# Kernel tuning notes

Hardware: AMD Instinct MI355X
Metric: run time of the kernel (lower is better)

The kernel has to match this reference:

```python
import jax, jax.numpy as jnp
import numpy as np

N_NODES = 64000
N_GRAPHS = 128


def _sage_conv(x, edge_index, Wl, Wr, b):
    # PyG SAGEConv (mean aggregator): out = lin_l(mean_{j in N(i)} x_j) + lin_r(x_i)
    src, dst = edge_index[0], edge_index[1]
    msg = x[src]                                   # [E, d] gather
    s = jax.ops.segment_sum(msg, dst, num_segments=N_NODES)          # [N, d]
    cnt = jax.ops.segment_sum(jnp.ones(src.shape, x.dtype), dst,
                              num_segments=N_NODES)[:, None]          # [N, 1]
    aggr = jnp.where(cnt > 0, s / jnp.maximum(cnt, 1.0), jnp.zeros((), x.dtype))
    return aggr @ Wl.T + x @ Wr.T + b


def setup_inputs() -> dict:
    key = jax.random.key(0)
    ks = jax.random.split(key, 9)
    E = 1024000
    x = jax.random.normal(ks[0], (N_NODES, 64), dtype=jnp.float32)
    edge_index = jax.random.randint(ks[1], (2, E), 0, N_NODES, dtype=jnp.int64)
    batch = jnp.sort(jax.random.randint(ks[2], (N_NODES,), 0, N_GRAPHS, dtype=jnp.int64))
    sc = 1.0 / np.sqrt(64.0)
    Wl = jax.random.normal(ks[3], (3, 64, 64), dtype=jnp.float32) * sc
    Wr = jax.random.normal(ks[4], (3, 64, 64), dtype=jnp.float32) * sc
    b = jax.random.normal(ks[5], (3, 64), dtype=jnp.float32) * sc
    Wl_out = jax.random.normal(ks[6], (2, 64), dtype=jnp.float32) * sc
    Wr_out = jax.random.normal(ks[7], (2, 64), dtype=jnp.float32) * sc
    b_out = jax.random.normal(ks[8], (2,), dtype=jnp.float32) * sc
    return {"x": x, "edge_index": edge_index, "batch": batch,
            "Wl": Wl, "Wr": Wr, "b": b,
            "Wl_out": Wl_out, "Wr_out": Wr_out, "b_out": b_out}


def reference(x, edge_index, batch, Wl, Wr, b, Wl_out, Wr_out, b_out):
    h = x
    for i in range(Wl.shape[0]):  # fixed n_layers=3 hidden SAGEConv layers
        h = _sage_conv(h, edge_index, Wl[i], Wr[i], b[i])
        # dropout is identity at inference
        h = jax.nn.relu(h)
    h = _sage_conv(h, edge_index, Wl_out, Wr_out, b_out)  # [N, n_classes]
    # global mean pool over graphs in the batch
    s = jax.ops.segment_sum(h, batch, num_segments=N_GRAPHS)
    cnt = jax.ops.segment_sum(jnp.ones((N_NODES,), h.dtype), batch,
                              num_segments=N_GRAPHS)[:, None]
    return s / jnp.maximum(cnt, 1.0)
```

## Files before the change

### kernel.cpp

```cpp
#include <hip/hip_runtime.h>

#define NNODES 64000
#define NGRAPHS 128
#define D 64
#define NT 250
#define ESEG 5120

typedef _Float16 half8 __attribute__((ext_vector_type(8)));
typedef float f32x4 __attribute__((ext_vector_type(4)));

__device__ __forceinline__ int lower_bound(const int* __restrict__ a, int n, int key) {
    int lo = 0, hi = n;
    while (lo < hi) {
        int mid = (lo + hi) >> 1;
        if (a[mid] < key) lo = mid + 1; else hi = mid;
    }
    return lo;
}


__global__ void tohalf_kernel(const float4* __restrict__ x, half8* __restrict__ xh, int n8,
                              const float* __restrict__ Wl, const float* __restrict__ Wr,
                              _Float16* __restrict__ Wlh, _Float16* __restrict__ Wrh) {
    int i = blockIdx.x * blockDim.x + threadIdx.x;
    int st = gridDim.x * blockDim.x;
    for (; i < n8; i += st) {
        float4 a = x[2 * i], b = x[2 * i + 1];
        half8 o;
        o[0] = (_Float16)a.x; o[1] = (_Float16)a.y; o[2] = (_Float16)a.z; o[3] = (_Float16)a.w;
        o[4] = (_Float16)b.x; o[5] = (_Float16)b.y; o[6] = (_Float16)b.z; o[7] = (_Float16)b.w;
        xh[i] = o;
    }
    int j = blockIdx.x * blockDim.x + threadIdx.x;
    if (j < 3 * D * D) {
        Wlh[j] = (_Float16)Wl[j];
        Wrh[j] = (_Float16)Wr[j];
    }
}

__global__ __launch_bounds__(256) void partition_kernel(
        const int* __restrict__ src, const int* __restrict__ dst, int E,
        int* __restrict__ ecur, int2* __restrict__ elist) {
    __shared__ int bcnt[256], bbase[256];
    const int U = 8;
    int tid = threadIdx.x;
    for (int base = blockIdx.x * 256 * U; base < E; base += gridDim.x * 256 * U) {
        bcnt[tid] = 0;
        __syncthreads();
        int2 ed[U]; int team[U], slot[U];
#pragma unroll
        for (int u = 0; u < U; ++u) {
            int e = base + tid + u * 256;
            team[u] = -1;
            if (e < E) {
                int s = __builtin_nontemporal_load(src + e);
                int d = __builtin_nontemporal_load(dst + e);
                ed[u] = make_int2(s, d);
                team[u] = d >> 8;
                slot[u] = atomicAdd(&bcnt[team[u]], 1);
            }
        }
        __syncthreads();
        if (bcnt[tid] > 0) bbase[tid] = atomicAdd(&ecur[tid], bcnt[tid]);
        __syncthreads();
#pragma unroll
        for (int u = 0; u < U; ++u)
            if (team[u] >= 0)
                elist[(size_t)team[u] * ESEG + bbase[team[u]] + slot[u]] = ed[u];
        __syncthreads();
    }
}

__global__ void teamscan_kernel(const int* __restrict__ ecur, int* __restrict__ tbase,
                                int* __restrict__ offs) {
    __shared__ int s[256];
    int t = threadIdx.x;
    int v = (t < NT) ? ecur[t] : 0;
    s[t] = v;
    __syncthreads();
    for (int off = 1; off < 256; off <<= 1) {
        int x = (t >= off) ? s[t - off] : 0;
        __syncthreads();
        s[t] += x;
        __syncthreads();
    }
    if (t < NT) tbase[t] = s[t] - v;
    if (t == 255) offs[NNODES] = s[255];
}

__global__ __launch_bounds__(1024) void fill_block(
        const int2* __restrict__ elist, const int* __restrict__ ecur,
        const int* __restrict__ tbase, const int* __restrict__ batch,
        int* __restrict__ offs, int2* __restrict__ info, int* __restrict__ col) {
    __shared__ int lhist[256], lofs[256];
    int team = blockIdx.x;
    int t = threadIdx.x;
    int n = ecur[team];
    int tb = tbase[team];
    const int2* el = elist + (size_t)team * ESEG;
    if (t < 256) lhist[t] = 0;
    __syncthreads();
    for (int e = t; e < n; e += 1024)
        atomicAdd(&lhist[el[e].y & 255], 1);
    __syncthreads();
    if (t < 256) lofs[t] = lhist[t];
    __syncthreads();
    for (int off = 1; off < 256; off <<= 1) {
        int x = 0;
        if (t < 256 && t >= off) x = lofs[t - off];
        __syncthreads();
        if (t < 256) lofs[t] += x;
        __syncthreads();
    }
    if (t < 256) {
        int v = lhist[t];
        int ex = lofs[t] - v;
        int gi = team * 256 + t;
        offs[gi] = tb + ex;
        float inv = (v > 0) ? 1.f / (float)v : 0.f;
        info[gi] = make_int2(batch[gi], __float_as_int(inv));
        lofs[t] = ex;
    }
    __syncthreads();
    for (int e = t; e < n; e += 1024) {
        int2 ed = el[e];
        int p = tb + atomicAdd(&lofs[ed.y & 255], 1);
        col[p] = ed.x;
    }
}

template <int PRJ>
__global__ __launch_bounds__(256) void layer_fused(
        const _Float16* __restrict__ h, _Float16* __restrict__ out,
        const int* __restrict__ offs, const int* __restrict__ col,
        const _Float16* __restrict__ Wlh, const _Float16* __restrict__ Wrh,
        const float* __restrict__ b,
        const float* __restrict__ Wlo, const float* __restrict__ Wro,
        float* __restrict__ z12, float* __restrict__ z34) {
    __shared__ _Float16 tile[4][16][D];
    int lane = threadIdx.x & 63;
    int w    = threadIdx.x >> 6;
    int row0 = (blockIdx.x * 4 + w) * 16;

    int ns = lane >> 3;
    int ch = lane & 7;
#pragma unroll
    for (int pass = 0; pass < 2; ++pass) {
        int i = row0 + pass * 8 + ns;
        int beg = offs[i], end = offs[i + 1];
        float s[8] = {0.f, 0.f, 0.f, 0.f, 0.f, 0.f, 0.f, 0.f};
        int e = beg;
        for (; e + 8 <= end; e += 8) {
            int c[8];
#pragma unroll
            for (int u = 0; u < 8; ++u) c[u] = col[e + u];
            half8 v[8];
#pragma unroll
            for (int u = 0; u < 8; ++u)
                v[u] = *(const half8*)(h + (size_t)c[u] * D + ch * 8);
#pragma unroll
            for (int u = 0; u < 8; ++u)
#pragma unroll
                for (int j = 0; j < 8; ++j) s[j] += (float)v[u][j];
        }
        for (; e + 4 <= end; e += 4) {
            int c0 = col[e], c1 = col[e + 1], c2 = col[e + 2], c3 = col[e + 3];
            half8 v0 = *(const half8*)(h + (size_t)c0 * D + ch * 8);
            half8 v1 = *(const half8*)(h + (size_t)c1 * D + ch * 8);
            half8 v2 = *(const half8*)(h + (size_t)c2 * D + ch * 8);
            half8 v3 = *(const half8*)(h + (size_t)c3 * D + ch * 8);
#pragma unroll
            for (int j = 0; j < 8; ++j)
                s[j] += ((float)v0[j] + (float)v1[j]) + ((float)v2[j] + (float)v3[j]);
        }
        for (; e < end; ++e) {
            half8 v = *(const half8*)(h + (size_t)col[e] * D + ch * 8);
#pragma unroll
            for (int j = 0; j < 8; ++j) s[j] += (float)v[j];
        }
        float inv = (end > beg) ? 1.f / (float)(end - beg) : 0.f;
        half8 o;
#pragma unroll
        for (int j = 0; j < 8; ++j) o[j] = (_Float16)(s[j] * inv);
        *(half8*)(&tile[w][pass * 8 + ns][ch * 8]) = o;
    }

    int r = lane & 15;
    int g = lane >> 4;

    half8 bf[4][4];
#pragma unroll
    for (int kt = 0; kt < 4; ++kt) {
        const _Float16* Wm = (kt < 2) ? Wlh : Wrh;
        int kk = (kt & 1) * 32 + g * 8;
#pragma unroll
        for (int nt = 0; nt < 4; ++nt)
            bf[kt][nt] = *(const half8*)(Wm + (size_t)(nt * 16 + r) * D + kk);
    }

    f32x4 acc[4];
#pragma unroll
    for (int nt = 0; nt < 4; ++nt) {
        float bv = b[nt * 16 + r];
        acc[nt] = (f32x4){bv, bv, bv, bv};
    }

#pragma unroll
    for (int kt = 0; kt < 4; ++kt) {
        int kk = (kt & 1) * 32 + g * 8;
        half8 af;
        if (kt < 2) af = *(const half8*)(&tile[w][r][kk]);
        else        af = *(const half8*)(h + (size_t)(row0 + r) * D + kk);
#pragma unroll
        for (int nt = 0; nt < 4; ++nt)
            acc[nt] = __builtin_amdgcn_mfma_f32_16x16x32_f16(af, bf[kt][nt], acc[nt], 0, 0, 0);
    }

    if (!PRJ) {
#pragma unroll
        for (int nt = 0; nt < 4; ++nt)
#pragma unroll
            for (int q = 0; q < 4; ++q) {
                int row = row0 + g * 4 + q;
                out[(size_t)row * D + nt * 16 + r] = (_Float16)fmaxf(acc[nt][q], 0.f);
            }
    } else {
#pragma unroll
        for (int nt = 0; nt < 4; ++nt)
#pragma unroll
            for (int q = 0; q < 4; ++q)
                tile[w][g * 4 + q][nt * 16 + r] = (_Float16)fmaxf(acc[nt][q], 0.f);

        half8 pf[2];
#pragma unroll
        for (int kt = 0; kt < 2; ++kt) {
            half8 t = {0, 0, 0, 0, 0, 0, 0, 0};
            if (r < 4) {
                const float* Pr = (r < 2) ? (Wlo + r * D) : (Wro + (r - 2) * D);
                int kk = kt * 32 + g * 8;
#pragma unroll
                for (int j = 0; j < 8; ++j) t[j] = (_Float16)Pr[kk + j];
            }
            pf[kt] = t;
        }
        f32x4 az = (f32x4){0.f, 0.f, 0.f, 0.f};
#pragma unroll
        for (int kt = 0; kt < 2; ++kt) {
            half8 af = *(const half8*)(&tile[w][r][kt * 32 + g * 8]);
            az = __builtin_amdgcn_mfma_f32_16x16x32_f16(af, pf[kt], az, 0, 0, 0);
        }
#pragma unroll
        for (int q = 0; q < 4; ++q) {
            int row = row0 + g * 4 + q;
            if (r < 2)      z12[row * 2 + r]       = az[q];
            else if (r < 4) z34[row * 2 + (r - 2)] = az[q];
        }
    }
}

__global__ __launch_bounds__(256) void zpool_edge(
        const float2* __restrict__ z12, const float2* __restrict__ z34,
        const int* __restrict__ src, const int* __restrict__ dst,
        const int2* __restrict__ info, int E, float* __restrict__ pool) {
    __shared__ float lp[NGRAPHS * 2];
    int t = threadIdx.x;
    lp[t] = 0.f;
    __syncthreads();
    int tid = blockIdx.x * blockDim.x + t;
    int stride = gridDim.x * blockDim.x;
    for (int e = tid; e < E; e += stride) {
        int s = __builtin_nontemporal_load(src + e);
        int d = __builtin_nontemporal_load(dst + e);
        float2 z = z12[s];
        int2 nf = info[d];
        float w = __int_as_float(nf.y);
        atomicAdd(&lp[nf.x * 2 + 0], z.x * w);
        atomicAdd(&lp[nf.x * 2 + 1], z.y * w);
    }
    for (int i = tid; i < NNODES; i += stride) {
        float2 zi = z34[i];
        int g = info[i].x;
        atomicAdd(&lp[g * 2 + 0], zi.x);
        atomicAdd(&lp[g * 2 + 1], zi.y);
    }
    __syncthreads();
    float v = lp[t];
    if (v != 0.f) atomicAdd(&pool[t], v);
}

__global__ void out_kernel(const float* __restrict__ pool, const int* __restrict__ batch,
                           const float* __restrict__ bo, float* __restrict__ out) {
    int t = threadIdx.x;
    int g = t >> 1, j = t & 1;
    int start = lower_bound(batch, NNODES, g);
    int end   = lower_bound(batch, NNODES, g + 1);
    int c = end - start;
    out[t] = (c > 0) ? pool[t] / (float)c + bo[j] : 0.f;
}


extern "C" void kernel_launch(void* const* d_in, const int* in_sizes, int n_in,
                              void* d_out, int out_size, void* d_ws, size_t ws_size,
                              hipStream_t stream) {
    const float* x    = (const float*)d_in[0];
    const int*   eidx = (const int*)d_in[1];
    const int*   batch= (const int*)d_in[2];
    const float* Wl   = (const float*)d_in[3];
    const float* Wr   = (const float*)d_in[4];
    const float* b    = (const float*)d_in[5];
    const float* Wlo  = (const float*)d_in[6];
    const float* Wro  = (const float*)d_in[7];
    const float* bo   = (const float*)d_in[8];

    int E = in_sizes[1] / 2;
    const int* src = eidx;
    const int* dst = eidx + E;

    char* ws = (char*)d_ws;
    size_t hb = (size_t)NNODES * D * 2;
    _Float16* xh   = (_Float16*)ws;
    _Float16* bufA = (_Float16*)(ws + hb);
    char* p = ws + 2 * hb;
    _Float16* Wlh  = (_Float16*)p;  p += 3 * D * D * 2;
    _Float16* Wrh  = (_Float16*)p;  p += 3 * D * D * 2;
    int*    col  = (int*)p;     p += (size_t)E * 4;
    int*    offs = (int*)p;     p += ((size_t)(NNODES + 1) * 4 + 127) / 128 * 128;
    int2*   info = (int2*)p;    p += (size_t)NNODES * 8;
    float*  z12  = (float*)p;   p += (size_t)NNODES * 8;
    float*  z34  = (float*)p;   p += (size_t)NNODES * 8;
    float*  pool = (float*)p;   p += (size_t)NGRAPHS * 2 * 4 + 64;
    int*    ecur = (int*)p;     p += 1024;
    int*    tbase= (int*)p;     p += 1024;
    int2*   elist= (int2*)p;

    hipMemsetAsync(pool, 0, NGRAPHS * 2 * sizeof(float), stream);
    hipMemsetAsync(ecur, 0, NT * sizeof(int), stream);

    tohalf_kernel<<<2000, 256, 0, stream>>>((const float4*)x, (half8*)xh, NNODES * D / 8,
                                            Wl, Wr, Wlh, Wrh);

    partition_kernel<<<512, 256, 0, stream>>>(src, dst, E, ecur, elist);
    teamscan_kernel<<<1, 256, 0, stream>>>(ecur, tbase, offs);
    fill_block<<<NT, 1024, 0, stream>>>(elist, ecur, tbase, batch, offs, info, col);

    layer_fused<0><<<1000, 256, 0, stream>>>(xh,   bufA, offs, col,
                                             Wlh,             Wrh,             b,
                                             nullptr, nullptr, nullptr, nullptr);
    layer_fused<0><<<1000, 256, 0, stream>>>(bufA, xh,   offs, col,
                                             Wlh + D * D,     Wrh + D * D,     b + D,
                                             nullptr, nullptr, nullptr, nullptr);
    layer_fused<1><<<1000, 256, 0, stream>>>(xh,   bufA, offs, col,
                                             Wlh + 2 * D * D, Wrh + 2 * D * D, b + 2 * D,
                                             Wlo, Wro, z12, z34);

    zpool_edge<<<1024, 256, 0, stream>>>((const float2*)z12, (const float2*)z34,
                                         src, dst, info, E, pool);
    out_kernel<<<1, 256, 0, stream>>>(pool, batch, bo, (float*)d_out);
}
```

Measured before the change: 170.3 us.

## Drop memsets and scan kernel, accumulate gathers in fp16, deterministic pool partials

The two memsets are removed: the zeroing of the team counters moves into the tohalf kernel. The separate team-scan kernel is folded into fill_block, where each block redoes the 250-entry scan. Neighbour aggregation in the layer kernel now sums in packed fp16 vectors instead of converting every element to fp32, cutting ALU work in the gather loop but adding rounding and overflow risk for high-degree nodes. zpool_edge now runs with 512 blocks, each writing its partial sums to a buffer that out_kernel reduces serially, replacing the global atomics.

```diff
diff --git a/kernel.cpp b/kernel.cpp
--- a/kernel.cpp
+++ b/kernel.cpp
@@ -5,6 +5,7 @@
 #define D 64
 #define NT 250
 #define ESEG 5120
+#define ZG 512
 
 typedef _Float16 half8 __attribute__((ext_vector_type(8)));
 typedef float f32x4 __attribute__((ext_vector_type(4)));
@@ -21,7 +22,8 @@
 
 __global__ void tohalf_kernel(const float4* __restrict__ x, half8* __restrict__ xh, int n8,
                               const float* __restrict__ Wl, const float* __restrict__ Wr,
-                              _Float16* __restrict__ Wlh, _Float16* __restrict__ Wrh) {
+                              _Float16* __restrict__ Wlh, _Float16* __restrict__ Wrh,
+                              int* __restrict__ ecur) {
     int i = blockIdx.x * blockDim.x + threadIdx.x;
     int st = gridDim.x * blockDim.x;
     for (; i < n8; i += st) {
@@ -36,6 +38,7 @@
         Wlh[j] = (_Float16)Wl[j];
         Wrh[j] = (_Float16)Wr[j];
     }
+    if (blockIdx.x == 0 && threadIdx.x < 256) ecur[threadIdx.x] = 0;
 }
 
 __global__ __launch_bounds__(256) void partition_kernel(
@@ -71,33 +74,29 @@
     }
 }
 
-__global__ void teamscan_kernel(const int* __restrict__ ecur, int* __restrict__ tbase,
-                                int* __restrict__ offs) {
-    __shared__ int s[256];
-    int t = threadIdx.x;
-    int v = (t < NT) ? ecur[t] : 0;
-    s[t] = v;
-    __syncthreads();
-    for (int off = 1; off < 256; off <<= 1) {
-        int x = (t >= off) ? s[t - off] : 0;
-        __syncthreads();
-        s[t] += x;
-        __syncthreads();
-    }
-    if (t < NT) tbase[t] = s[t] - v;
-    if (t == 255) offs[NNODES] = s[255];
-}
-
 __global__ __launch_bounds__(1024) void fill_block(
         const int2* __restrict__ elist, const int* __restrict__ ecur,
-        const int* __restrict__ tbase, const int* __restrict__ batch,
+        const int* __restrict__ batch,
         int* __restrict__ offs, int2* __restrict__ info, int* __restrict__ col) {
     __shared__ int lhist[256], lofs[256];
     int team = blockIdx.x;
     int t = threadIdx.x;
     int n = ecur[team];
-    int tb = tbase[team];
     const int2* el = elist + (size_t)team * ESEG;
+
+    if (t < 256) lofs[t] = (t < NT) ? ecur[t] : 0;
+    __syncthreads();
+    for (int off = 1; off < 256; off <<= 1) {
+        int x = 0;
+        if (t < 256 && t >= off) x = lofs[t - off];
+        __syncthreads();
+        if (t < 256) lofs[t] += x;
+        __syncthreads();
+    }
+    int tb = (team > 0) ? lofs[team - 1] : 0;
+    if (team == NT - 1 && t == 0) offs[NNODES] = lofs[NT - 1];
+    __syncthreads();
+
     if (t < 256) lhist[t] = 0;
     __syncthreads();
     for (int e = t; e < n; e += 1024)
@@ -148,7 +147,7 @@
     for (int pass = 0; pass < 2; ++pass) {
         int i = row0 + pass * 8 + ns;
         int beg = offs[i], end = offs[i + 1];
-        float s[8] = {0.f, 0.f, 0.f, 0.f, 0.f, 0.f, 0.f, 0.f};
+        half8 sa = {0, 0, 0, 0, 0, 0, 0, 0};
         int e = beg;
         for (; e + 8 <= end; e += 8) {
             int c[8];
@@ -158,10 +157,9 @@
 #pragma unroll
             for (int u = 0; u < 8; ++u)
                 v[u] = *(const half8*)(h + (size_t)c[u] * D + ch * 8);
-#pragma unroll
-            for (int u = 0; u < 8; ++u)
-#pragma unroll
-                for (int j = 0; j < 8; ++j) s[j] += (float)v[u][j];
+            half8 t0 = v[0] + v[1], t1 = v[2] + v[3];
+            half8 t2 = v[4] + v[5], t3 = v[6] + v[7];
+            sa += (t0 + t1) + (t2 + t3);
         }
         for (; e + 4 <= end; e += 4) {
             int c0 = col[e], c1 = col[e + 1], c2 = col[e + 2], c3 = col[e + 3];
@@ -169,19 +167,14 @@
             half8 v1 = *(const half8*)(h + (size_t)c1 * D + ch * 8);
             half8 v2 = *(const half8*)(h + (size_t)c2 * D + ch * 8);
             half8 v3 = *(const half8*)(h + (size_t)c3 * D + ch * 8);
-#pragma unroll
-            for (int j = 0; j < 8; ++j)
-                s[j] += ((float)v0[j] + (float)v1[j]) + ((float)v2[j] + (float)v3[j]);
-        }
-        for (; e < end; ++e) {
-            half8 v = *(const half8*)(h + (size_t)col[e] * D + ch * 8);
-#pragma unroll
-            for (int j = 0; j < 8; ++j) s[j] += (float)v[j];
-        }
+            sa += (v0 + v1) + (v2 + v3);
+        }
+        for (; e < end; ++e)
+            sa += *(const half8*)(h + (size_t)col[e] * D + ch * 8);
         float inv = (end > beg) ? 1.f / (float)(end - beg) : 0.f;
         half8 o;
 #pragma unroll
-        for (int j = 0; j < 8; ++j) o[j] = (_Float16)(s[j] * inv);
+        for (int j = 0; j < 8; ++j) o[j] = (_Float16)((float)sa[j] * inv);
         *(half8*)(&tile[w][pass * 8 + ns][ch * 8]) = o;
     }
 
@@ -261,7 +254,7 @@
 __global__ __launch_bounds__(256) void zpool_edge(
         const float2* __restrict__ z12, const float2* __restrict__ z34,
         const int* __restrict__ src, const int* __restrict__ dst,
-        const int2* __restrict__ info, int E, float* __restrict__ pool) {
+        const int2* __restrict__ info, int E, float* __restrict__ pbuf) {
     __shared__ float lp[NGRAPHS * 2];
     int t = threadIdx.x;
     lp[t] = 0.f;
@@ -284,18 +277,19 @@
         atomicAdd(&lp[g * 2 + 1], zi.y);
     }
     __syncthreads();
-    float v = lp[t];
-    if (v != 0.f) atomicAdd(&pool[t], v);
-}
-
-__global__ void out_kernel(const float* __restrict__ pool, const int* __restrict__ batch,
+    pbuf[blockIdx.x * (NGRAPHS * 2) + t] = lp[t];
+}
+
+__global__ void out_kernel(const float* __restrict__ pbuf, const int* __restrict__ batch,
                            const float* __restrict__ bo, float* __restrict__ out) {
     int t = threadIdx.x;
+    float s = 0.f;
+    for (int k = 0; k < ZG; ++k) s += pbuf[k * (NGRAPHS * 2) + t];
     int g = t >> 1, j = t & 1;
     int start = lower_bound(batch, NNODES, g);
     int end   = lower_bound(batch, NNODES, g + 1);
     int c = end - start;
-    out[t] = (c > 0) ? pool[t] / (float)c + bo[j] : 0.f;
+    out[t] = (c > 0) ? s / (float)c + bo[j] : 0.f;
 }
 
 
@@ -328,20 +322,15 @@
     int2*   info = (int2*)p;    p += (size_t)NNODES * 8;
     float*  z12  = (float*)p;   p += (size_t)NNODES * 8;
     float*  z34  = (float*)p;   p += (size_t)NNODES * 8;
-    float*  pool = (float*)p;   p += (size_t)NGRAPHS * 2 * 4 + 64;
     int*    ecur = (int*)p;     p += 1024;
-    int*    tbase= (int*)p;     p += 1024;
+    float*  pbuf = (float*)p;   p += (size_t)ZG * NGRAPHS * 2 * 4;
     int2*   elist= (int2*)p;
 
-    hipMemsetAsync(pool, 0, NGRAPHS * 2 * sizeof(float), stream);
-    hipMemsetAsync(ecur, 0, NT * sizeof(int), stream);
-
     tohalf_kernel<<<2000, 256, 0, stream>>>((const float4*)x, (half8*)xh, NNODES * D / 8,
-                                            Wl, Wr, Wlh, Wrh);
+                                            Wl, Wr, Wlh, Wrh, ecur);
 
     partition_kernel<<<512, 256, 0, stream>>>(src, dst, E, ecur, elist);
-    teamscan_kernel<<<1, 256, 0, stream>>>(ecur, tbase, offs);
-    fill_block<<<NT, 1024, 0, stream>>>(elist, ecur, tbase, batch, offs, info, col);
+    fill_block<<<NT, 1024, 0, stream>>>(elist, ecur, batch, offs, info, col);
 
     layer_fused<0><<<1000, 256, 0, stream>>>(xh,   bufA, offs, col,
                                              Wlh,             Wrh,             b,
@@ -353,7 +342,7 @@
                                              Wlh + 2 * D * D, Wrh + 2 * D * D, b + 2 * D,
                                              Wlo, Wro, z12, z34);
 
-    zpool_edge<<<1024, 256, 0, stream>>>((const float2*)z12, (const float2*)z34,
-                                         src, dst, info, E, pool);
-    out_kernel<<<1, 256, 0, stream>>>(pool, batch, bo, (float*)d_out);
-}
+    zpool_edge<<<ZG, 256, 0, stream>>>((const float2*)z12, (const float2*)z34,
+                                       src, dst, info, E, pbuf);
+    out_kernel<<<1, 256, 0, stream>>>(pbuf, batch, bo, (float*)d_out);
+}
```

New measurement: 151.6 us. -11.0%, faster.
